# Optimization experiments

Hardware: AMD Instinct MI355X
Metric: run time of the kernel (lower is better)

Reference implementation:

```python
import jax, jax.numpy as jnp
import numpy as np

CONTEXT = 5
PAD = CONTEXT // 2
EPS = 1e-12  # torch F.normalize eps


def _conv2d(x, w, b):
    # x: [B,Cin,H,W], w: [Cout,Cin,3,3], SAME padding (pad=1)
    y = jax.lax.conv_general_dilated(
        x, w, window_strides=(1, 1), padding='SAME',
        dimension_numbers=('NCHW', 'OIHW', 'NCHW'))
    return y + b[None, :, None, None]


def _self_similarity(fn):
    # fn: L2-normalized features [B,C,H,W] -> cost volume [B,25,H,W]
    b, c, h, w = fn.shape
    fp = jnp.pad(fn, ((0, 0), (0, 0), (PAD, PAD), (PAD, PAD)))
    # channel index = col*CONTEXT + row, matching the torch loop order
    planes = [
        (fp[:, :, r:h + r, cc:w + cc] * fn).sum(axis=1)
        for cc in range(CONTEXT) for r in range(CONTEXT)
    ]
    return jnp.stack(planes, axis=1)


def setup_inputs() -> dict:
    key = jax.random.key(0)
    ks = jax.random.split(key, 5)
    B, C, H, W = 8, 512, 96, 96
    OC = 128
    return {
        'feature': jax.random.normal(ks[0], (B, C, H, W), dtype=jnp.float32),
        'w0': jax.random.normal(ks[1], (2 * OC, CONTEXT * CONTEXT, 3, 3), dtype=jnp.float32) * 0.05,
        'b0': jax.random.normal(ks[2], (2 * OC,), dtype=jnp.float32) * 0.01,
        'w1': jax.random.normal(ks[3], (OC, 2 * OC, 3, 3), dtype=jnp.float32) * 0.05,
        'b1': jax.random.normal(ks[4], (OC,), dtype=jnp.float32) * 0.01,
    }


def reference(feature, w0, b0, w1, b1):
    # F.normalize(p=2, dim=1): divide by channel L2 norm clamped to eps
    norm = jnp.sqrt((feature * feature).sum(axis=1, keepdims=True))
    fn = feature / jnp.maximum(norm, EPS)
    ss = _self_similarity(fn)                 # [B,25,H,W]
    ss1 = jax.nn.relu(_conv2d(ss, w0, b0))    # [B,256,H,W]
    ss2 = jax.nn.relu(_conv2d(ss1, w1, b1))   # [B,128,H,W]
    return jnp.concatenate((ss, ss1, ss2), axis=1)  # [B,409,H,W]
```

## Files before the change

kernel.cpp:

```cpp
#include <hip/hip_runtime.h>

#define FEAT_C 512
#define Hh 96
#define Ww 96
#define HW (Hh*Ww)
#define NB 8
#define OUTC 409

typedef __attribute__((ext_vector_type(8))) short short8;
typedef __attribute__((ext_vector_type(4))) short short4v;
typedef __attribute__((ext_vector_type(4))) float f32x4;
typedef __fp16 h2 __attribute__((ext_vector_type(2)));
typedef __fp16 h8 __attribute__((ext_vector_type(8)));

typedef __attribute__((address_space(1))) const unsigned int gu32;
typedef __attribute__((address_space(3))) unsigned int lu32;

#define VMCNT(N) do { asm volatile("s_waitcnt vmcnt(" #N ")" ::: "memory"); \
                      __builtin_amdgcn_sched_barrier(0); } while (0)
#define LGKM0()  do { asm volatile("s_waitcnt lgkmcnt(0)" ::: "memory"); \
                      __builtin_amdgcn_sched_barrier(0); } while (0)

__device__ inline ushort f2bf(float x) {
    unsigned u = __float_as_uint(x);
    u += 0x7fffu + ((u >> 16) & 1u);
    return (ushort)(u >> 16);
}

#if __has_builtin(__builtin_amdgcn_fdot2)
__device__ inline float FDOT2(h2 a, h2 b, float c) {
    return __builtin_amdgcn_fdot2(a, b, c, false);
}
#else
__device__ inline float FDOT2(h2 a, h2 b, float c) {
    return c + (float)a[0] * (float)b[0] + (float)a[1] * (float)b[1];
}
#endif

__device__ inline h2 pair(h8 v, int i) {
    switch (i) {
        case 0: return __builtin_shufflevector(v, v, 0, 1);
        case 1: return __builtin_shufflevector(v, v, 2, 3);
        case 2: return __builtin_shufflevector(v, v, 4, 5);
        default: return __builtin_shufflevector(v, v, 6, 7);
    }
}

#define PKPX 32
__global__ __launch_bounds__(256) void kpack(const float* __restrict__ f,
                                             ushort* __restrict__ fnorm) {
    __shared__ ushort tr[PKPX * 512];
    __shared__ float ssqp[8][PKPX];
    __shared__ float sinvs[PKPX];
    int tid = threadIdx.x;
    int g = tid >> 5, pl = tid & 31;
    int b = blockIdx.y;
    int p0 = blockIdx.x * PKPX;
    const float* fb = f + (size_t)b * FEAT_C * HW + p0 + pl;

    float ssq = 0.f;
#pragma unroll
    for (int q = 0; q < 8; ++q) {
        int u = g * 8 + q;
        float v[8];
#pragma unroll
        for (int j = 0; j < 8; ++j)
            v[j] = fb[(size_t)(u * 8 + j) * HW];
        h2 a0 = __builtin_amdgcn_cvt_pkrtz(v[0], v[1]);
        h2 a1 = __builtin_amdgcn_cvt_pkrtz(v[2], v[3]);
        h2 a2 = __builtin_amdgcn_cvt_pkrtz(v[4], v[5]);
        h2 a3 = __builtin_amdgcn_cvt_pkrtz(v[6], v[7]);
        ssq = FDOT2(a0, a0, ssq); ssq = FDOT2(a1, a1, ssq);
        ssq = FDOT2(a2, a2, ssq); ssq = FDOT2(a3, a3, ssq);
        h8 hv;
        hv[0] = a0[0]; hv[1] = a0[1]; hv[2] = a1[0]; hv[3] = a1[1];
        hv[4] = a2[0]; hv[5] = a2[1]; hv[6] = a3[0]; hv[7] = a3[1];
        int up = u ^ (pl & 7);
        *(h8*)&tr[pl * 512 + up * 8] = hv;
    }
    ssqp[g][pl] = ssq;
    __syncthreads();
    if (tid < PKPX) {
        float s = 0.f;
#pragma unroll
        for (int gg = 0; gg < 8; ++gg) s += ssqp[gg][tid];
        sinvs[tid] = 1.0f / fmaxf(sqrtf(s), 1e-12f);
    }
    __syncthreads();

    size_t ob = ((size_t)b * HW + p0) * 512;
#pragma unroll
    for (int i = 0; i < 8; ++i) {
        int t = tid + i * 256;
        int r = t >> 6, k = t & 63;
        h8 hv = *(const h8*)&tr[r * 512 + ((k ^ (r & 7)) * 8)];
        float s = sinvs[r];
        h2 o0 = __builtin_amdgcn_cvt_pkrtz((float)hv[0] * s, (float)hv[1] * s);
        h2 o1 = __builtin_amdgcn_cvt_pkrtz((float)hv[2] * s, (float)hv[3] * s);
        h2 o2 = __builtin_amdgcn_cvt_pkrtz((float)hv[4] * s, (float)hv[5] * s);
        h2 o3 = __builtin_amdgcn_cvt_pkrtz((float)hv[6] * s, (float)hv[7] * s);
        h8 ov;
        ov[0] = o0[0]; ov[1] = o0[1]; ov[2] = o1[0]; ov[3] = o1[1];
        ov[4] = o2[0]; ov[5] = o2[1]; ov[6] = o3[0]; ov[7] = o3[1];
        *(h8*)&fnorm[ob + (size_t)r * 512 + k * 8] = ov;
    }
}

#define SS_NPX 240
__global__ __launch_bounds__(256) void kss4(const ushort* __restrict__ fnorm,
                                            float* __restrict__ out,
                                            ushort* __restrict__ sspk0) {
    __shared__ ushort tile[2][SS_NPX * 32];
    int tid = threadIdx.x;
    int w = tid >> 6, lane = tid & 63;
    int s = lane >> 4, q = lane & 15;
    int x0 = blockIdx.x * 16, y0 = blockIdx.y * 8, b = blockIdx.z;

    size_t t_src[4];
    int t_dst[4];
    bool t_ok[4];
#pragma unroll
    for (int k = 0; k < 4; ++k) {
        int task = tid + k * 256;
        t_ok[k] = false; t_src[k] = 0; t_dst[k] = -1;
        if (task < 960) {
            int px = task >> 2, u = task & 3;
            int hr = px / 20, hc = px % 20;
            int gy = y0 + hr - 2, gx = x0 + hc - 2;
            t_dst[k] = px * 32 + ((u ^ ((px >> 1) & 3)) * 8);
            if (gy >= 0 && gy < Hh && gx >= 0 && gx < Ww) {
                t_ok[k] = true;
                t_src[k] = ((size_t)b * HW + (size_t)gy * Ww + gx) * 512 + u * 8;
            }
        }
    }

    float acc0[25], acc1[25];
#pragma unroll
    for (int o = 0; o < 25; ++o) { acc0[o] = 0.f; acc1[o] = 0.f; }

    auto stage = [&](int chunk, int nbuf) {
        short8 v[4];
#pragma unroll
        for (int k = 0; k < 4; ++k) {
            v[k] = (short8)0;
            if (t_ok[k]) v[k] = *(const short8*)(fnorm + t_src[k] + chunk * 32);
        }
#pragma unroll
        for (int k = 0; k < 4; ++k)
            if (t_dst[k] >= 0)
                *(short8*)&tile[nbuf][t_dst[k]] = v[k];
    };

    auto compute = [&](int kb) {
        const ushort* tb = tile[kb];
        auto rd = [&](int px) -> h8 {
            return *(const h8*)&tb[px * 32 + ((s ^ ((px >> 1) & 3)) * 8)];
        };
        int pc0 = (2 * w + 2) * 20 + q + 2;
        h8 c0 = rd(pc0);
        h8 c1 = rd(pc0 + 20);
#pragma unroll
        for (int dxc = 0; dxc < 5; ++dxc) {
#pragma unroll
            for (int dyr = 0; dyr < 6; ++dyr) {
                int pn = (2 * w + dyr) * 20 + q + dxc;
                h8 nv = rd(pn);
                if (dyr < 5) {
                    float a = acc0[dxc * 5 + dyr];
                    a = FDOT2(pair(nv, 0), pair(c0, 0), a);
                    a = FDOT2(pair(nv, 1), pair(c0, 1), a);
                    a = FDOT2(pair(nv, 2), pair(c0, 2), a);
                    a = FDOT2(pair(nv, 3), pair(c0, 3), a);
                    acc0[dxc * 5 + dyr] = a;
                }
                if (dyr > 0) {
                    float a = acc1[dxc * 5 + dyr - 1];
                    a = FDOT2(pair(nv, 0), pair(c1, 0), a);
                    a = FDOT2(pair(nv, 1), pair(c1, 1), a);
                    a = FDOT2(pair(nv, 2), pair(c1, 2), a);
                    a = FDOT2(pair(nv, 3), pair(c1, 3), a);
                    acc1[dxc * 5 + dyr - 1] = a;
                }
            }
        }
    };

    stage(0, 0);
    __syncthreads();
    for (int c = 0; c < 16; ++c) {
        if (c < 15) stage(c + 1, (c + 1) & 1);
        compute(c & 1);
        __syncthreads();
    }

#pragma unroll
    for (int o = 0; o < 25; ++o) {
        float v0 = acc0[o];
        v0 += __shfl_xor(v0, 16);
        v0 += __shfl_xor(v0, 32);
        acc0[o] = v0;
        float v1 = acc1[o];
        v1 += __shfl_xor(v1, 16);
        v1 += __shfl_xor(v1, 32);
        acc1[o] = v1;
    }
    if (s == 0) {
        int gy0 = y0 + 2 * w, gx = x0 + q;
        size_t pix0 = (size_t)b * HW + (size_t)gy0 * Ww + gx;
        size_t ob0 = (size_t)b * OUTC * HW + (size_t)gy0 * Ww + gx;
#pragma unroll
        for (int o = 0; o < 25; ++o) {
            out[ob0 + (size_t)o * HW] = acc0[o];
            out[ob0 + (size_t)o * HW + Ww] = acc1[o];
        }
        ushort pk0[32], pk1[32];
#pragma unroll
        for (int o = 0; o < 25; ++o) { pk0[o] = f2bf(acc0[o]); pk1[o] = f2bf(acc1[o]); }
#pragma unroll
        for (int o = 25; o < 32; ++o) { pk0[o] = 0; pk1[o] = 0; }
#pragma unroll
        for (int u = 0; u < 4; ++u) {
            *(short8*)&sspk0[pix0 * 32 + u * 8] = *(short8*)&pk0[u * 8];
            *(short8*)&sspk0[(pix0 + Ww) * 32 + u * 8] = *(short8*)&pk1[u * 8];
        }
    }
}

__global__ __launch_bounds__(256) void kwpack0(const float* __restrict__ w0,
                                               ushort* __restrict__ wpk0) {
    int i = blockIdx.x * 256 + threadIdx.x;
    if (i >= 9 * 256 * 32) return;
    int t = i >> 13, oc = (i >> 5) & 255;
    int s = (i >> 3) & 3, ii = i & 7;
    int u = s ^ ((oc >> 1) & 3);
    int ic = u * 8 + ii;
    wpk0[i] = (ic < 25) ? f2bf(w0[(size_t)oc * 225 + ic * 9 + t]) : (ushort)0;
}

__global__ __launch_bounds__(256) void kwpack1(const float* __restrict__ w1,
                                               ushort* __restrict__ wpk1,
                                               ushort* __restrict__ zpad) {
    if (blockIdx.x == 0 && threadIdx.x < 32) zpad[threadIdx.x] = 0;
    int i = blockIdx.x * 256 + threadIdx.x;
    if (i >= 8 * 9 * 128 * 32) return;
    int ct = i >> 12;
    int c = ct / 9, t = ct % 9;
    int oc = (i >> 5) & 127;
    int s = (i >> 3) & 3, ii = i & 7;
    int u = s ^ ((oc >> 1) & 3);
    int ic = c * 32 + u * 8 + ii;
    wpk1[i] = f2bf(w1[((size_t)oc * 256 + ic) * 9 + t]);
}

#define C1NPX 180
__global__ __launch_bounds__(512, 2) void kconv1m(const ushort* __restrict__ sspk0,
                                                  const ushort* __restrict__ wpk0,
                                                  const float* __restrict__ b0,
                                                  float* __restrict__ outp,
                                                  ushort* __restrict__ sspk) {
    __shared__ ushort plds[C1NPX * 32];
    int tid = threadIdx.x;
    int lane = tid & 63, wid = tid >> 6;
    int wM = wid >> 1, wN = wid & 1;
    int l15 = lane & 15, l4 = lane >> 4;
    int x0 = blockIdx.x * 16, y0 = blockIdx.y * 8, b = blockIdx.z;

    short8 pv[2]; int pdst[2];
#pragma unroll
    for (int k = 0; k < 2; ++k) {
        int task = tid + k * 512;
        pv[k] = (short8)0; pdst[k] = -1;
        if (task < 720) {
            int px = task >> 2, u = task & 3;
            int iy = px / 18, ix = px % 18;
            int gy = y0 + iy - 1, gx = x0 + ix - 1;
            pdst[k] = px * 32 + (u ^ ((px >> 1) & 3)) * 8;
            if (gy >= 0 && gy < Hh && gx >= 0 && gx < Ww)
                pv[k] = *(const short8*)(sspk0 +
                        ((size_t)b * HW + (size_t)gy * Ww + gx) * 32 + u * 8);
        }
    }

    int wslot = l4 ^ ((l15 >> 1) & 3);
    const ushort* abase = wpk0 + (size_t)(wM * 64 + l15) * 32 + wslot * 8;
    short8 sA[4], sB[4];
    auto aload = [&](int t, short8 (&S)[4]) {
#pragma unroll
        for (int mi = 0; mi < 4; ++mi)
            S[mi] = *(const short8*)(abase + (size_t)t * 8192 + mi * 512);
    };

    aload(0, sA);
    aload(1, sB);

#pragma unroll
    for (int k = 0; k < 2; ++k)
        if (pdst[k] >= 0) *(short8*)&plds[pdst[k]] = pv[k];
    LGKM0();
    __builtin_amdgcn_s_barrier();

    f32x4 acc[4][4];
#pragma unroll
    for (int mi = 0; mi < 4; ++mi)
#pragma unroll
        for (int ni = 0; ni < 4; ++ni)
            acc[mi][ni] = (f32x4)0.f;

    auto compute = [&](const short8 (&S)[4], int ky, int kx) {
        short8 bv[4];
#pragma unroll
        for (int ni = 0; ni < 4; ++ni) {
            int ipx = (wN * 4 + ni + ky) * 18 + l15 + kx;
            bv[ni] = *(const short8*)&plds[ipx * 32
                    + ((l4 ^ ((ipx >> 1) & 3)) * 8)];
        }
#pragma unroll
        for (int mi = 0; mi < 4; ++mi)
#pragma unroll
            for (int ni = 0; ni < 4; ++ni)
                acc[mi][ni] = __builtin_amdgcn_mfma_f32_16x16x32_bf16(
                    S[mi], bv[ni], acc[mi][ni], 0, 0, 0);
    };

#pragma unroll
    for (int t = 0; t < 9; ++t) {
        if (t < 8) { VMCNT(4); } else { VMCNT(0); }
        int ky = t / 3, kx = t % 3;
        if ((t & 1) == 0) {
            compute(sA, ky, kx);
            if (t < 7) aload(t + 2, sA);
        } else {
            compute(sB, ky, kx);
            if (t < 7) aload(t + 2, sB);
        }
    }

    size_t ob = (size_t)b * OUTC * HW + (size_t)25 * HW;
    size_t pb = (size_t)b * HW;
#pragma unroll
    for (int mi = 0; mi < 4; ++mi)
#pragma unroll
        for (int ni = 0; ni < 4; ++ni) {
            int gy = y0 + wN * 4 + ni, gx = x0 + l15;
            int oc_b = wM * 64 + mi * 16 + l4 * 4;
            short4v hv;
#pragma unroll
            for (int r = 0; r < 4; ++r) {
                float v = fmaxf(acc[mi][ni][r] + b0[oc_b + r], 0.f);
                outp[ob + (size_t)(oc_b + r) * HW + (size_t)gy * Ww + gx] = v;
                hv[r] = (short)f2bf(v);
            }
            *(short4v*)&sspk[(pb + (size_t)gy * Ww + gx) * 256 + oc_b] = hv;
        }
}

#define NPX2 180
__global__ __launch_bounds__(256, 2) void kconv2n(const ushort* __restrict__ sspk,
                                                  const ushort* __restrict__ wpk,
                                                  const float* __restrict__ b1,
                                                  const ushort* __restrict__ zpad,
                                                  float* __restrict__ outp) {
    __shared__ ushort plds[2][6144];
    int tid = threadIdx.x;
    int lane = tid & 63, wid = tid >> 6;
    int wM = wid >> 1, wN = wid & 1;
    int l15 = lane & 15, l4 = lane >> 4;
    int x0 = blockIdx.x * 16, y0 = blockIdx.y * 8, b = blockIdx.z;

    f32x4 acc[4][4];
#pragma unroll
    for (int mi = 0; mi < 4; ++mi)
#pragma unroll
        for (int ni = 0; ni < 4; ++ni)
            acc[mi][ni] = (f32x4)0.f;

    const ushort* p_src[3];
    int p_ok[3];
#pragma unroll
    for (int k = 0; k < 3; ++k) {
        int task = tid + k * 256;
        int px = task >> 2, slot = task & 3;
        int u = slot ^ ((px >> 1) & 3);
        int iy = px / 18, ix = px % 18;
        int gy = y0 + iy - 1, gx = x0 + ix - 1;
        bool ok = (px < NPX2) && gy >= 0 && gy < Hh && gx >= 0 && gx < Ww;
        p_ok[k] = ok ? 1 : 0;
        p_src[k] = ok ? (sspk + ((size_t)b * HW + (size_t)gy * Ww + gx) * 256
                         + u * 8)
                      : zpad;
    }
    auto pstage = [&](int c, int buf) {
#pragma unroll
        for (int k = 0; k < 3; ++k)
            __builtin_amdgcn_global_load_lds(
                (gu32*)(p_src[k] + (p_ok[k] ? c * 32 : 0)),
                (lu32*)&plds[buf][(k * 256 + wid * 64) * 8], 16, 0, 0);
    };

    int wslot = l4 ^ ((l15 >> 1) & 3);
    const ushort* abase = wpk + (size_t)(wM * 64 + l15) * 32 + wslot * 8;
    short8 sA[12], sB[12];
    auto aload = [&](int g, short8 (&S)[12]) {
#pragma unroll
        for (int kx = 0; kx < 3; ++kx)
#pragma unroll
            for (int mi = 0; mi < 4; ++mi)
                S[kx * 4 + mi] = *(const short8*)(abase + (size_t)g * 12288
                                                  + kx * 4096 + mi * 512);
    };
    auto compute = [&](const short8 (&S)[12], const ushort* lbase, int ky) {
#pragma unroll
        for (int kx = 0; kx < 3; ++kx) {
            short8 bv[4];
#pragma unroll
            for (int ni = 0; ni < 4; ++ni) {
                int oy = wN * 4 + ni;
                int ipx = (oy + ky) * 18 + l15 + kx;
                bv[ni] = *(const short8*)&lbase[ipx * 32
                        + ((l4 ^ ((ipx >> 1) & 3)) * 8)];
            }
#pragma unroll
            for (int mi = 0; mi < 4; ++mi)
#pragma unroll
                for (int ni = 0; ni < 4; ++ni)
                    acc[mi][ni] = __builtin_amdgcn_mfma_f32_16x16x32_bf16(
                        S[kx * 4 + mi], bv[ni], acc[mi][ni], 0, 0, 0);
        }
    };

    auto chunk = [&](int c, short8 (&Scur)[12], short8 (&Salt)[12], bool last) {
        const ushort* lbase = plds[c & 1];
        VMCNT(12);
        __builtin_amdgcn_s_barrier();
        compute(Scur, lbase, 0);
        aload(3 * c + 2, Scur);
        VMCNT(12);
        compute(Salt, lbase, 1);
        if (!last) {
            aload(3 * c + 3, Salt);
            pstage(c + 1, (c + 1) & 1);
            VMCNT(15);
        } else {
            VMCNT(0);
        }
        compute(Scur, lbase, 2);
        if (!last) aload(3 * c + 4, Scur);
    };

    pstage(0, 0);
    aload(0, sA);
    aload(1, sB);

    for (int c2 = 0; c2 < 4; ++c2) {
        chunk(2 * c2,     sA, sB, false);
        chunk(2 * c2 + 1, sB, sA, c2 == 3);
    }

    size_t ob = (size_t)b * OUTC * HW + (size_t)281 * HW;
#pragma unroll
    for (int mi = 0; mi < 4; ++mi)
#pragma unroll
        for (int ni = 0; ni < 4; ++ni) {
            int gy = y0 + wN * 4 + ni, gx = x0 + l15;
#pragma unroll
            for (int r = 0; r < 4; ++r) {
                int oc = wM * 64 + mi * 16 + l4 * 4 + r;
                float v = acc[mi][ni][r] + b1[oc];
                outp[ob + (size_t)oc * HW + (size_t)gy * Ww + gx] = fmaxf(v, 0.f);
            }
        }
}

extern "C" void kernel_launch(void* const* d_in, const int* in_sizes, int n_in,
                              void* d_out, int out_size, void* d_ws, size_t ws_size,
                              hipStream_t stream) {
    const float* feat = (const float*)d_in[0];
    const float* w0   = (const float*)d_in[1];
    const float* b0   = (const float*)d_in[2];
    const float* w1   = (const float*)d_in[3];
    const float* b1   = (const float*)d_in[4];
    float* out = (float*)d_out;

    ushort* wpk0  = (ushort*)d_ws;
    ushort* wpk1  = (ushort*)((char*)d_ws + 147456);
    ushort* sspk  = (ushort*)((char*)d_ws + 147456 + 589824);
    ushort* fnorm = (ushort*)((char*)d_ws + 147456 + 589824 + 37748736);
    ushort* sspk0 = (ushort*)((char*)d_ws + 147456 + 589824 + 37748736
                              + 75497472);
    ushort* zpad  = (ushort*)((char*)d_ws + 147456 + 589824 + 37748736
                              + 75497472 + 4718592);

    hipLaunchKernelGGL(kwpack0, dim3(288),  dim3(256), 0, stream, w0, wpk0);
    hipLaunchKernelGGL(kwpack1, dim3(1152), dim3(256), 0, stream, w1, wpk1, zpad);
    hipLaunchKernelGGL(kpack,   dim3(HW / PKPX, NB), dim3(256), 0, stream, feat, fnorm);
    hipLaunchKernelGGL(kss4,    dim3(6, 12, NB), dim3(256), 0, stream, fnorm, out, sspk0);
    hipLaunchKernelGGL(kconv1m, dim3(6, 12, NB), dim3(512), 0, stream, sspk0, wpk0, b0, out, sspk);
    hipLaunchKernelGGL(kconv2n, dim3(6, 12, NB), dim3(256), 0, stream, sspk, wpk1, b1, zpad, out);
}
```

Measured before the change: 191.8 us.

## Split conv2 K dimension across waves with LDS reduction; fuse weight-pack kernels

The conv2 kernel now splits the 256 input channels between two wave groups (wK), so each wave holds 4x8 accumulator tiles covering all 8 output rows. Each step stages two channel chunks into a doubled LDS buffer. The partial sums are then reduced through LDS before bias, ReLU and the store. This halves the weight loads per wave and raises B-fragment reuse, at the cost of more accumulator registers, more LDS and an extra reduction phase. Separately, the two weight-packing kernels are merged into one launch to cut launch overhead.

```diff
diff --git a/kernel.cpp b/kernel.cpp
--- a/kernel.cpp
+++ b/kernel.cpp
@@ -227,30 +227,31 @@
     }
 }
 
-__global__ __launch_bounds__(256) void kwpack0(const float* __restrict__ w0,
-                                               ushort* __restrict__ wpk0) {
-    int i = blockIdx.x * 256 + threadIdx.x;
-    if (i >= 9 * 256 * 32) return;
-    int t = i >> 13, oc = (i >> 5) & 255;
-    int s = (i >> 3) & 3, ii = i & 7;
-    int u = s ^ ((oc >> 1) & 3);
-    int ic = u * 8 + ii;
-    wpk0[i] = (ic < 25) ? f2bf(w0[(size_t)oc * 225 + ic * 9 + t]) : (ushort)0;
-}
-
-__global__ __launch_bounds__(256) void kwpack1(const float* __restrict__ w1,
+__global__ __launch_bounds__(256) void kwpacks(const float* __restrict__ w0,
+                                               const float* __restrict__ w1,
+                                               ushort* __restrict__ wpk0,
                                                ushort* __restrict__ wpk1,
                                                ushort* __restrict__ zpad) {
     if (blockIdx.x == 0 && threadIdx.x < 32) zpad[threadIdx.x] = 0;
-    int i = blockIdx.x * 256 + threadIdx.x;
-    if (i >= 8 * 9 * 128 * 32) return;
-    int ct = i >> 12;
-    int c = ct / 9, t = ct % 9;
-    int oc = (i >> 5) & 127;
-    int s = (i >> 3) & 3, ii = i & 7;
-    int u = s ^ ((oc >> 1) & 3);
-    int ic = c * 32 + u * 8 + ii;
-    wpk1[i] = f2bf(w1[((size_t)oc * 256 + ic) * 9 + t]);
+    if (blockIdx.x < 288) {
+        int i = blockIdx.x * 256 + threadIdx.x;
+        if (i >= 9 * 256 * 32) return;
+        int t = i >> 13, oc = (i >> 5) & 255;
+        int s = (i >> 3) & 3, ii = i & 7;
+        int u = s ^ ((oc >> 1) & 3);
+        int ic = u * 8 + ii;
+        wpk0[i] = (ic < 25) ? f2bf(w0[(size_t)oc * 225 + ic * 9 + t]) : (ushort)0;
+    } else {
+        int i = (blockIdx.x - 288) * 256 + threadIdx.x;
+        if (i >= 8 * 9 * 128 * 32) return;
+        int ct = i >> 12;
+        int c = ct / 9, t = ct % 9;
+        int oc = (i >> 5) & 127;
+        int s = (i >> 3) & 3, ii = i & 7;
+        int u = s ^ ((oc >> 1) & 3);
+        int ic = c * 32 + u * 8 + ii;
+        wpk1[i] = f2bf(w1[((size_t)oc * 256 + ic) * 9 + t]);
+    }
 }
 
 #define C1NPX 180
@@ -361,18 +362,18 @@
                                                   const float* __restrict__ b1,
                                                   const ushort* __restrict__ zpad,
                                                   float* __restrict__ outp) {
-    __shared__ ushort plds[2][6144];
+    __shared__ ushort plds[2][12288];
     int tid = threadIdx.x;
     int lane = tid & 63, wid = tid >> 6;
-    int wM = wid >> 1, wN = wid & 1;
+    int wM = wid & 1, wK = wid >> 1;
     int l15 = lane & 15, l4 = lane >> 4;
     int x0 = blockIdx.x * 16, y0 = blockIdx.y * 8, b = blockIdx.z;
 
-    f32x4 acc[4][4];
+    f32x4 acc[4][8];
 #pragma unroll
     for (int mi = 0; mi < 4; ++mi)
 #pragma unroll
-        for (int ni = 0; ni < 4; ++ni)
+        for (int ni = 0; ni < 8; ++ni)
             acc[mi][ni] = (f32x4)0.f;
 
     const ushort* p_src[3];
@@ -395,81 +396,112 @@
         for (int k = 0; k < 3; ++k)
             __builtin_amdgcn_global_load_lds(
                 (gu32*)(p_src[k] + (p_ok[k] ? c * 32 : 0)),
-                (lu32*)&plds[buf][(k * 256 + wid * 64) * 8], 16, 0, 0);
+                (lu32*)&plds[buf][(c >> 2) * 6144 + (k * 256 + wid * 64) * 8],
+                16, 0, 0);
     };
 
     int wslot = l4 ^ ((l15 >> 1) & 3);
-    const ushort* abase = wpk + (size_t)(wM * 64 + l15) * 32 + wslot * 8;
+    const ushort* abase = wpk + (size_t)(wK * 12) * 12288
+                        + (size_t)(wM * 64 + l15) * 32 + wslot * 8;
     short8 sA[12], sB[12];
-    auto aload = [&](int g, short8 (&S)[12]) {
+    auto aload = [&](int r, short8 (&S)[12]) {
 #pragma unroll
         for (int kx = 0; kx < 3; ++kx)
 #pragma unroll
             for (int mi = 0; mi < 4; ++mi)
-                S[kx * 4 + mi] = *(const short8*)(abase + (size_t)g * 12288
+                S[kx * 4 + mi] = *(const short8*)(abase + (size_t)r * 12288
                                                   + kx * 4096 + mi * 512);
     };
     auto compute = [&](const short8 (&S)[12], const ushort* lbase, int ky) {
 #pragma unroll
         for (int kx = 0; kx < 3; ++kx) {
-            short8 bv[4];
-#pragma unroll
-            for (int ni = 0; ni < 4; ++ni) {
-                int oy = wN * 4 + ni;
-                int ipx = (oy + ky) * 18 + l15 + kx;
+            short8 bv[8];
+#pragma unroll
+            for (int ni = 0; ni < 8; ++ni) {
+                int ipx = (ni + ky) * 18 + l15 + kx;
                 bv[ni] = *(const short8*)&lbase[ipx * 32
                         + ((l4 ^ ((ipx >> 1) & 3)) * 8)];
             }
 #pragma unroll
             for (int mi = 0; mi < 4; ++mi)
 #pragma unroll
-                for (int ni = 0; ni < 4; ++ni)
+                for (int ni = 0; ni < 8; ++ni)
                     acc[mi][ni] = __builtin_amdgcn_mfma_f32_16x16x32_bf16(
                         S[kx * 4 + mi], bv[ni], acc[mi][ni], 0, 0, 0);
         }
     };
 
-    auto chunk = [&](int c, short8 (&Scur)[12], short8 (&Salt)[12], bool last) {
-        const ushort* lbase = plds[c & 1];
+    auto tstep = [&](int t, short8 (&Scur)[12], short8 (&Salt)[12], bool last) {
+        const ushort* lbase = &plds[t & 1][wK * 6144];
+        int r = 3 * t;
         VMCNT(12);
         __builtin_amdgcn_s_barrier();
         compute(Scur, lbase, 0);
-        aload(3 * c + 2, Scur);
+        aload(r + 2, Scur);
         VMCNT(12);
         compute(Salt, lbase, 1);
         if (!last) {
-            aload(3 * c + 3, Salt);
-            pstage(c + 1, (c + 1) & 1);
-            VMCNT(15);
+            aload(r + 3, Salt);
+            pstage(t + 1, (t + 1) & 1);
+            pstage(t + 5, (t + 1) & 1);
+            VMCNT(18);
         } else {
             VMCNT(0);
         }
         compute(Scur, lbase, 2);
-        if (!last) aload(3 * c + 4, Scur);
+        if (!last) aload(r + 4, Scur);
     };
 
     pstage(0, 0);
+    pstage(4, 0);
     aload(0, sA);
     aload(1, sB);
 
-    for (int c2 = 0; c2 < 4; ++c2) {
-        chunk(2 * c2,     sA, sB, false);
-        chunk(2 * c2 + 1, sB, sA, c2 == 3);
-    }
-
+    tstep(0, sA, sB, false);
+    tstep(1, sB, sA, false);
+    tstep(2, sA, sB, false);
+    tstep(3, sB, sA, true);
+
+    float* red = (float*)plds;
     size_t ob = (size_t)b * OUTC * HW + (size_t)281 * HW;
-#pragma unroll
-    for (int mi = 0; mi < 4; ++mi)
-#pragma unroll
-        for (int ni = 0; ni < 4; ++ni) {
-            int gy = y0 + wN * 4 + ni, gx = x0 + l15;
-#pragma unroll
-            for (int r = 0; r < 4; ++r) {
-                int oc = wM * 64 + mi * 16 + l4 * 4 + r;
-                float v = acc[mi][ni][r] + b1[oc];
-                outp[ob + (size_t)oc * HW + (size_t)gy * Ww + gx] = fmaxf(v, 0.f);
+    LGKM0();
+    __builtin_amdgcn_s_barrier();
+#pragma unroll
+    for (int p = 0; p < 2; ++p) {
+        if (wK == 1) {
+#pragma unroll
+            for (int mh = 0; mh < 2; ++mh) {
+                int mi = p * 2 + mh;
+#pragma unroll
+                for (int ni = 0; ni < 8; ++ni)
+                    *(f32x4*)&red[wM * 4096 + mh * 2048 + ni * 256 + lane * 4]
+                        = acc[mi][ni];
             }
         }
+        LGKM0();
+        __builtin_amdgcn_s_barrier();
+        if (wK == 0) {
+#pragma unroll
+            for (int mh = 0; mh < 2; ++mh) {
+                int mi = p * 2 + mh;
+#pragma unroll
+                for (int ni = 0; ni < 8; ++ni) {
+                    f32x4 other = *(const f32x4*)&red[wM * 4096 + mh * 2048
+                                                     + ni * 256 + lane * 4];
+                    int gy = y0 + ni, gx = x0 + l15;
+                    int oc_b = wM * 64 + mi * 16 + l4 * 4;
+#pragma unroll
+                    for (int r = 0; r < 4; ++r) {
+                        float v = acc[mi][ni][r] + other[r] + b1[oc_b + r];
+                        outp[ob + (size_t)(oc_b + r) * HW + (size_t)gy * Ww + gx]
+                            = fmaxf(v, 0.f);
+                    }
+                }
+            }
+        }
+        LGKM0();
+        __builtin_amdgcn_s_barrier();
+    }
 }
 
 extern "C" void kernel_launch(void* const* d_in, const int* in_sizes, int n_in,
@@ -491,8 +523,7 @@
     ushort* zpad  = (ushort*)((char*)d_ws + 147456 + 589824 + 37748736
                               + 75497472 + 4718592);
 
-    hipLaunchKernelGGL(kwpack0, dim3(288),  dim3(256), 0, stream, w0, wpk0);
-    hipLaunchKernelGGL(kwpack1, dim3(1152), dim3(256), 0, stream, w1, wpk1, zpad);
+    hipLaunchKernelGGL(kwpacks, dim3(1440), dim3(256), 0, stream, w0, w1, wpk0, wpk1, zpad);
     hipLaunchKernelGGL(kpack,   dim3(HW / PKPX, NB), dim3(256), 0, stream, feat, fnorm);
     hipLaunchKernelGGL(kss4,    dim3(6, 12, NB), dim3(256), 0, stream, fnorm, out, sspk0);
     hipLaunchKernelGGL(kconv1m, dim3(6, 12, NB), dim3(512), 0, stream, sspk0, wpk0, b0, out, sspk);
```

After: 289.1 us. 50.7% more time.
